# Optimization experiments

Hardware: AMD Instinct MI355X
Metric: run time of the kernel (lower is better)

The kernel has to match this reference:

```python
import jax, jax.numpy as jnp
import numpy as np

B, C, L = 4, 64, 4096
RED = 4          # reduction -> q/k channels = C // RED = 16
N_HASHES = 4
HASH_BUCKETS = min(L // 4, 32)  # = 32, matches torch code
EPS = 1e-5


def _conv1x1(x, W, b):
    # x: [B, Cin, L], W: [Cout, Cin], b: [Cout]
    return jnp.einsum('bcl,oc->bol', x, W) + b[None, :, None]


def setup_inputs() -> dict:
    key = jax.random.key(0)
    ks = jax.random.split(key, 12)
    Cq = C // RED
    x = jax.random.normal(ks[0], (B, C, L), dtype=jnp.float32)
    hash_idx = jax.random.randint(ks[1], (B, N_HASHES, L), 0, HASH_BUCKETS, dtype=jnp.int32)
    sC = 1.0 / np.sqrt(C)
    Wq = jax.random.normal(ks[2], (Cq, C), dtype=jnp.float32) * sC
    bq = jax.random.normal(ks[3], (Cq,), dtype=jnp.float32) * 0.01
    Wk = jax.random.normal(ks[4], (Cq, C), dtype=jnp.float32) * sC
    bk = jax.random.normal(ks[5], (Cq,), dtype=jnp.float32) * 0.01
    Wv = jax.random.normal(ks[6], (C, C), dtype=jnp.float32) * sC
    bv = jax.random.normal(ks[7], (C,), dtype=jnp.float32) * 0.01
    Wo = jax.random.normal(ks[8], (C, C), dtype=jnp.float32) * sC
    bo = jax.random.normal(ks[9], (C,), dtype=jnp.float32) * 0.01
    gamma = jax.random.normal(ks[10], (1,), dtype=jnp.float32)  # nonzero so attn path matters
    bn_w = jnp.ones((C,), dtype=jnp.float32)
    bn_b = jnp.zeros((C,), dtype=jnp.float32)
    return dict(x=x, hash_idx=hash_idx, Wq=Wq, bq=bq, Wk=Wk, bk=bk,
                Wv=Wv, bv=bv, Wo=Wo, bo=bo, gamma=gamma, bn_w=bn_w, bn_b=bn_b)


def reference(x, hash_idx, Wq, bq, Wk, bk, Wv, bv, Wo, bo, gamma, bn_w, bn_b):
    # 1x1 conv projections
    q = _conv1x1(x, Wq, bq)   # [B, C/RED, L]
    k = _conv1x1(x, Wk, bk)   # [B, C/RED, L]
    v = _conv1x1(x, Wv, bv)   # [B, C, L]

    qT = q.transpose(0, 2, 1)  # [B, L, Cq]
    kT = k.transpose(0, 2, 1)
    vT = v.transpose(0, 2, 1)  # [B, L, C]

    # raw scores are hash-independent; only the bucket mask changes per hash
    scores = jnp.einsum('bic,bjc->bij', qT, kT)  # [B, L, L], no sqrt(d) scaling (matches torch)

    n_hashes = hash_idx.shape[1]
    acc = jnp.zeros_like(vT)
    for h in range(n_hashes):  # small fixed loop
        idx = hash_idx[:, h, :]                       # [B, L]
        mask = idx[:, :, None] == idx[:, None, :]     # same-bucket mask [B, L, L]
        s = jnp.where(mask, scores, -1e9)
        attn = jax.nn.softmax(s, axis=-1)             # within-bucket softmax (diag always valid)
        acc = acc + jnp.einsum('bij,bjc->bic', attn, vT)
    attn_out = (acc / n_hashes).transpose(0, 2, 1)    # [B, C, L], averaged over hashes

    out = _conv1x1(attn_out, Wo, bo)
    out = gamma * out + x                             # residual with learned scalar

    # BatchNorm1d, training mode: biased batch stats over (B, L) per channel
    mean = out.mean(axis=(0, 2), keepdims=True)
    var = out.var(axis=(0, 2), keepdims=True)
    out = (out - mean) * jax.lax.rsqrt(var + EPS)
    out = out * bn_w[None, :, None] + bn_b[None, :, None]
    return out
```

## Files before the change

### kernel.cpp

```cpp
#include <hip/hip_runtime.h>
#include <math.h>

#define Bn 4
#define Cn 64
#define Ln 4096
#define CQ 16
#define NH 4
#define NB 32
#define EPSV 1e-5f

#define MAXS 384
#define SFULL 192

#define QSZ   (Bn*Ln*CQ)
#define VSZ   (Bn*Ln*Cn)
#define ACCSZ (Bn*Ln*Cn)
#define NBH   (Bn*NH)

#define OFF_K   QSZ
#define OFF_V   (2*QSZ)
#define OFF_ACC (2*QSZ + VSZ)

#define LOG2E 1.44269504088896f

__global__ __launch_bounds__(256) void proj_kernel(
        const float* __restrict__ x,
        const float* __restrict__ Wq, const float* __restrict__ bq,
        const float* __restrict__ Wk, const float* __restrict__ bk,
        const float* __restrict__ Wv, const float* __restrict__ bv,
        float* __restrict__ q, float* __restrict__ k, float* __restrict__ v) {
    __shared__ float sWt[Cn*32];
    __shared__ float sb[32];
    int tid = threadIdx.x;
    int third = blockIdx.x % 3;
    int pg    = blockIdx.x / 3;
    int rbase = third * 32;
    for (int idx = tid; idx < Cn*32; idx += 256) {
        int rr = idx & 31, c = idx >> 5;
        int r = rbase + rr;
        float w;
        if (r < 16)      w = Wq[r*Cn + c];
        else if (r < 32) w = Wk[(r-16)*Cn + c];
        else             w = Wv[(r-32)*Cn + c];
        sWt[c*32 + rr] = w;
    }
    if (tid < 32) {
        int r = rbase + tid;
        sb[tid] = (r < 16) ? bq[r] : (r < 32 ? bk[r-16] : bv[r-32]);
    }
    __syncthreads();
    int p = tid & 63, og = tid >> 6;
    int gp = pg * 64 + p;
    int b = gp >> 12, l = gp & (Ln - 1);
    const float* xp = &x[b*Cn*Ln + l];
    int rr0 = og * 8;
    float val[8];
    #pragma unroll
    for (int i = 0; i < 8; i++) val[i] = sb[rr0 + i];
    #pragma unroll
    for (int c0 = 0; c0 < Cn; c0 += 8) {
        float xv[8];
        #pragma unroll
        for (int i = 0; i < 8; i++) xv[i] = xp[(c0 + i)*Ln];
        #pragma unroll
        for (int i = 0; i < 8; i++) {
            const float4 wa = *(const float4*)&sWt[(c0 + i)*32 + rr0];
            const float4 wb = *(const float4*)&sWt[(c0 + i)*32 + rr0 + 4];
            float xvi = xv[i];
            val[0] = fmaf(wa.x, xvi, val[0]); val[1] = fmaf(wa.y, xvi, val[1]);
            val[2] = fmaf(wa.z, xvi, val[2]); val[3] = fmaf(wa.w, xvi, val[3]);
            val[4] = fmaf(wb.x, xvi, val[4]); val[5] = fmaf(wb.y, xvi, val[5]);
            val[6] = fmaf(wb.z, xvi, val[6]); val[7] = fmaf(wb.w, xvi, val[7]);
        }
    }
    int f = third*8 + og*2;
    float4 t0 = make_float4(val[0], val[1], val[2], val[3]);
    float4 t1 = make_float4(val[4], val[5], val[6], val[7]);
    float4* q4 = (float4*)&q[gp*CQ];
    float4* k4 = (float4*)&k[gp*CQ];
    float4* v4 = (float4*)&v[gp*Cn];
    if (f < 4)      { q4[f]   = t0; q4[f+1] = t1; }
    else if (f < 8) { k4[f-4] = t0; k4[f-3] = t1; }
    else            { v4[f-8] = t0; v4[f-7] = t1; }
}

__device__ __forceinline__ float quad_reduce_sum(float d) {
    d += __int_as_float(__builtin_amdgcn_mov_dpp(__float_as_int(d), 0xB1, 0xF, 0xF, true));
    d += __int_as_float(__builtin_amdgcn_mov_dpp(__float_as_int(d), 0x4E, 0xF, 0xF, true));
    return d;
}

__device__ __forceinline__ float rowsum16(float x) {
    x += __int_as_float(__builtin_amdgcn_mov_dpp(__float_as_int(x), 0x114, 0xF, 0xF, true));
    x += __int_as_float(__builtin_amdgcn_mov_dpp(__float_as_int(x), 0x118, 0xF, 0xF, true));
    return x;
}

struct SweepState {
    float4 qr[4];
    float4 o[4][4];
    float  lsum[4];
    int    ir[4];
    int    qact[4];
};

__device__ __forceinline__ void sweep_init(SweepState& st, int q0, int S, int act,
        const int* list, const float4* Q4, int qq, int c4) {
    #pragma unroll
    for (int s = 0; s < 4; s++) {
        int qi = q0 + s*4 + qq;
        int a = act && (qi < S);
        st.qact[s] = a;
        int r = a ? list[qi] : 0;
        st.ir[s] = r;
        float4 t = make_float4(0.f, 0.f, 0.f, 0.f);
        if (a) {
            t = Q4[(size_t)r*4 + c4];
            t.x *= LOG2E; t.y *= LOG2E; t.z *= LOG2E; t.w *= LOG2E;
        }
        st.qr[s] = t;
        st.lsum[s] = 0.f;
        #pragma unroll
        for (int tt = 0; tt < 4; tt++) st.o[s][tt] = make_float4(0.f, 0.f, 0.f, 0.f);
    }
}

template<bool MASKED>
__device__ __forceinline__ void kb_step(SweepState& st, int kb, int nkv,
        const float4* ks4, const float4* vs4, int l15, int kk,
        int i0, int i1, int i2, int i3) {
    const float4 kq = ks4[kb*16 + l15];
    const float4 va = vs4[kb*64 + i0*16 + l15];
    const float4 vb = vs4[kb*64 + i1*16 + l15];
    const float4 vc = vs4[kb*64 + i2*16 + l15];
    const float4 vd = vs4[kb*64 + i3*16 + l15];
    #pragma unroll
    for (int s = 0; s < 4; s++) {
        float d = st.qr[s].x * kq.x;
        d = fmaf(st.qr[s].y, kq.y, d);
        d = fmaf(st.qr[s].z, kq.z, d);
        d = fmaf(st.qr[s].w, kq.w, d);
        d = quad_reduce_sum(d);
        float pw = __builtin_amdgcn_exp2f(d);
        if (MASKED) pw = ((kb*4 + kk) < nkv) ? pw : 0.f;
        st.lsum[s] += pw;
        st.o[s][0].x = fmaf(pw, va.x, st.o[s][0].x); st.o[s][0].y = fmaf(pw, va.y, st.o[s][0].y);
        st.o[s][0].z = fmaf(pw, va.z, st.o[s][0].z); st.o[s][0].w = fmaf(pw, va.w, st.o[s][0].w);
        st.o[s][1].x = fmaf(pw, vb.x, st.o[s][1].x); st.o[s][1].y = fmaf(pw, vb.y, st.o[s][1].y);
        st.o[s][1].z = fmaf(pw, vb.z, st.o[s][1].z); st.o[s][1].w = fmaf(pw, vb.w, st.o[s][1].w);
        st.o[s][2].x = fmaf(pw, vc.x, st.o[s][2].x); st.o[s][2].y = fmaf(pw, vc.y, st.o[s][2].y);
        st.o[s][2].z = fmaf(pw, vc.z, st.o[s][2].z); st.o[s][2].w = fmaf(pw, vc.w, st.o[s][2].w);
        st.o[s][3].x = fmaf(pw, vd.x, st.o[s][3].x); st.o[s][3].y = fmaf(pw, vd.y, st.o[s][3].y);
        st.o[s][3].z = fmaf(pw, vd.z, st.o[s][3].z); st.o[s][3].w = fmaf(pw, vd.w, st.o[s][3].w);
    }
}

__device__ __forceinline__ void sweep_keys(SweepState& st, int nk,
        const float4* ks4, const float4* vs4, int l15, int kk,
        int i0, int i1, int i2, int i3) {
    int nf = nk >> 2;
    for (int kb = 0; kb < nf; kb++)
        kb_step<false>(st, kb, nk, ks4, vs4, l15, kk, i0, i1, i2, i3);
    if (nk & 3)
        kb_step<true>(st, nf, nk, ks4, vs4, l15, kk, i0, i1, i2, i3);
}

template<int MODE>
__device__ __forceinline__ void sweep_fin(SweepState& st, float* __restrict__ acc,
        int b, int h, int qq, int lane, int c4) {
    #pragma unroll
    for (int s = 0; s < 4; s++) {
        st.lsum[s] = rowsum16(st.lsum[s]);
        #pragma unroll
        for (int t = 0; t < 4; t++) {
            st.o[s][t].x = rowsum16(st.o[s][t].x);
            st.o[s][t].y = rowsum16(st.o[s][t].y);
            st.o[s][t].z = rowsum16(st.o[s][t].z);
            st.o[s][t].w = rowsum16(st.o[s][t].w);
        }
    }
    if ((lane & 15) < 12) return;
    #pragma unroll
    for (int s = 0; s < 4; s++) {
        if (st.qact[s]) {
            float inv = 1.f / st.lsum[s];
            #pragma unroll
            for (int t = 0; t < 4; t++) {
                float4 r;
                r.x = st.o[s][t].x * inv; r.y = st.o[s][t].y * inv;
                r.z = st.o[s][t].z * inv; r.w = st.o[s][t].w * inv;
                int ch = ((qq + t) & 3)*16 + c4*4;
                if (MODE == 1) {
                    *(float4*)&acc[(((size_t)h*Bn + b)*Ln + st.ir[s])*Cn + ch] = r;
                } else {
                    float* ap = &acc[((size_t)b*Ln + st.ir[s])*Cn + ch];
                    atomicAdd(&ap[0], r.x); atomicAdd(&ap[1], r.y);
                    atomicAdd(&ap[2], r.z); atomicAdd(&ap[3], r.w);
                }
            }
        }
    }
}

__device__ __forceinline__ void stage_kv(int tid, int nk, int k0, const int* list,
        const float4* K4, const float4* V4, float4* ks4, float4* vs4) {
    const float4 z = make_float4(0.f, 0.f, 0.f, 0.f);
    int nb4 = (nk + 3) >> 2;
    for (int G = tid; G < nb4*16; G += 256) {
        int j = G >> 2;
        ks4[G] = (j < nk) ? K4[(size_t)list[k0 + j]*4 + (G & 3)] : z;
    }
    for (int F = tid; F < nb4*64; F += 256) {
        int kb = F >> 6, ii = (F >> 4) & 3, k2 = (F >> 2) & 3, cc = F & 3;
        int j = kb*4 + k2;
        vs4[F] = (j < nk) ? V4[(size_t)list[k0 + j]*16 + ii*4 + cc] : z;
    }
}

template<int MODE>
__global__ __launch_bounds__(256, 2) void attn_kernel(
        const float* __restrict__ q, const float* __restrict__ k,
        const float* __restrict__ v, const int* __restrict__ hidx,
        float* __restrict__ acc) {
    __shared__ int list[MAXS];
    __shared__ int wtot[4];
    __shared__ float4 ks4[SFULL*4];
    __shared__ float4 vs4[SFULL*16];
    int blk = blockIdx.x;
    int u  = blk & (NB-1);
    int bh = blk >> 5;
    int b  = bh >> 2;
    int h  = bh & 3;
    int tid = threadIdx.x;

    const int4* hp4 = (const int4*)(&hidx[bh*Ln] + tid*16);
    int hv[16];
    #pragma unroll
    for (int t = 0; t < 4; t++) {
        int4 tmp = hp4[t];
        hv[t*4+0]=tmp.x; hv[t*4+1]=tmp.y; hv[t*4+2]=tmp.z; hv[t*4+3]=tmp.w;
    }
    int myCnt = 0;
    #pragma unroll
    for (int t = 0; t < 16; t++) myCnt += (hv[t] == u);
    int lane = tid & 63, wv = tid >> 6;
    int pre = myCnt;
    #pragma unroll
    for (int d = 1; d < 64; d <<= 1) {
        int t = __shfl_up(pre, d, 64);
        if (lane >= d) pre += t;
    }
    if (lane == 63) wtot[wv] = pre;
    __syncthreads();
    int base = 0;
    #pragma unroll
    for (int w = 0; w < 4; w++) base += (w < wv) ? wtot[w] : 0;
    int Sall = wtot[0] + wtot[1] + wtot[2] + wtot[3];
    int S = min(Sall, MAXS);
    int excl = base + pre - myCnt;
    #pragma unroll
    for (int t = 0; t < 16; t++) {
        if (hv[t] == u) {
            if (excl < MAXS) list[excl] = tid*16 + t;
            excl++;
        }
    }
    __syncthreads();

    int qq = (lane >> 4) & 3;
    int kk = (lane >> 2) & 3;
    int c4 = lane & 3;
    int l15 = lane & 15;
    int i0 = qq, i1 = (qq+1)&3, i2 = (qq+2)&3, i3 = (qq+3)&3;
    const float4* Q4 = (const float4*)&q[(size_t)b*Ln*CQ];
    const float4* K4 = (const float4*)&k[(size_t)b*Ln*CQ];
    const float4* V4 = (const float4*)&v[(size_t)b*Ln*Cn];

    if (S <= SFULL) {
        stage_kv(tid, S, 0, list, K4, V4, ks4, vs4);
        __syncthreads();
        for (int q0 = wv*16; q0 < S; q0 += 64) {
            SweepState st;
            sweep_init(st, q0, S, 1, list, Q4, qq, c4);
            sweep_keys(st, S, ks4, vs4, l15, kk, i0, i1, i2, i3);
            sweep_fin<MODE>(st, acc, b, h, qq, lane, c4);
        }
    } else {
        for (int q0s = 0; q0s < S; q0s += 64) {
            int q0 = q0s + wv*16;
            int act = q0 < S;
            SweepState st;
            sweep_init(st, q0, S, act, list, Q4, qq, c4);
            for (int k0 = 0; k0 < S; k0 += SFULL) {
                int nk = min(SFULL, S - k0);
                __syncthreads();
                stage_kv(tid, nk, k0, list, K4, V4, ks4, vs4);
                __syncthreads();
                if (act) sweep_keys(st, nk, ks4, vs4, l15, kk, i0, i1, i2, i3);
            }
            if (act) sweep_fin<MODE>(st, acc, b, h, qq, lane, c4);
        }
    }
}

template<int MODE>
__global__ __launch_bounds__(256) void outconv_kernel(
        const float* __restrict__ acc, const float* __restrict__ Wo,
        const float* __restrict__ bo, const float* __restrict__ gamma,
        const float* __restrict__ x, float* __restrict__ y) {
    __shared__ float sWt[Cn*Cn];
    __shared__ float sA[Cn*33];
    __shared__ float sb[Cn];
    int tid = threadIdx.x;
    int pg = blockIdx.x;
    for (int idx = tid; idx < Cn*Cn; idx += 256) {
        int o = idx & 63, c = idx >> 6;
        sWt[c*Cn + o] = Wo[o*Cn + c];
    }
    if (tid < Cn) sb[tid] = bo[tid];
    const float4* a4 = (const float4*)&acc[(size_t)pg*32*Cn];
    #pragma unroll
    for (int r = 0; r < 2; r++) {
        int idx = r*256 + tid;
        int p = idx >> 4, c0 = (idx & 15) * 4;
        float4 t = a4[idx];
        if (MODE == 1) {
            float4 t1 = a4[(size_t)ACCSZ/4   + idx];
            float4 t2 = a4[(size_t)ACCSZ/4*2 + idx];
            float4 t3 = a4[(size_t)ACCSZ/4*3 + idx];
            t.x += t1.x + t2.x + t3.x; t.y += t1.y + t2.y + t3.y;
            t.z += t1.z + t2.z + t3.z; t.w += t1.w + t2.w + t3.w;
        }
        sA[(c0+0)*33 + p] = t.x*0.25f;
        sA[(c0+1)*33 + p] = t.y*0.25f;
        sA[(c0+2)*33 + p] = t.z*0.25f;
        sA[(c0+3)*33 + p] = t.w*0.25f;
    }
    __syncthreads();
    float g = gamma[0];
    int p = tid & 31, og = tid >> 5;
    int gp = pg * 32 + p;
    int b = gp >> 12, l = gp & (Ln - 1);
    int o0 = og * 8;
    float val[8];
    #pragma unroll
    for (int i = 0; i < 8; i++) val[i] = sb[o0 + i];
    #pragma unroll
    for (int c = 0; c < Cn; c++) {
        float av = sA[c*33 + p];
        const float4 wa = *(const float4*)&sWt[c*Cn + o0];
        const float4 wb = *(const float4*)&sWt[c*Cn + o0 + 4];
        val[0] = fmaf(wa.x, av, val[0]); val[1] = fmaf(wa.y, av, val[1]);
        val[2] = fmaf(wa.z, av, val[2]); val[3] = fmaf(wa.w, av, val[3]);
        val[4] = fmaf(wb.x, av, val[4]); val[5] = fmaf(wb.y, av, val[5]);
        val[6] = fmaf(wb.z, av, val[6]); val[7] = fmaf(wb.w, av, val[7]);
    }
    #pragma unroll
    for (int i = 0; i < 8; i++) {
        int o = o0 + i;
        float yv = fmaf(g, val[i], x[(b*Cn + o)*Ln + l]);
        y[(b*Cn + o)*Ln + l] = yv;
    }
}

__global__ __launch_bounds__(256) void stats_kernel(
        const float* __restrict__ y, float* __restrict__ ssumP, float* __restrict__ ssqP) {
    int c = blockIdx.x >> 2;
    int part = blockIdx.x & 3;
    int tid = threadIdx.x;
    const float4* yp = (const float4*)&y[(part*Cn + c)*Ln];
    float s = 0.f, s2 = 0.f;
    #pragma unroll
    for (int i = 0; i < 4; i++) {
        float4 t = yp[i*256 + tid];
        s  += t.x + t.y + t.z + t.w;
        s2 += t.x*t.x + t.y*t.y + t.z*t.z + t.w*t.w;
    }
    #pragma unroll
    for (int w = 1; w < 64; w <<= 1) {
        s  += __shfl_xor(s,  w, 64);
        s2 += __shfl_xor(s2, w, 64);
    }
    __shared__ float rs[4], rs2[4];
    int wv = tid >> 6;
    if ((tid & 63) == 0) { rs[wv] = s; rs2[wv] = s2; }
    __syncthreads();
    if (tid == 0) {
        ssumP[blockIdx.x] = rs[0]+rs[1]+rs[2]+rs[3];
        ssqP[blockIdx.x]  = rs2[0]+rs2[1]+rs2[2]+rs2[3];
    }
}

__global__ __launch_bounds__(256) void norm_kernel(
        const float* __restrict__ y,
        const float* __restrict__ ssumP, const float* __restrict__ ssqP,
        const float* __restrict__ bnw, const float* __restrict__ bnb,
        float* __restrict__ out) {
    int idx = blockIdx.x * 256 + threadIdx.x;
    int flat = idx * 4;
    int c = (flat / Ln) & 63;
    float s = 0.f, s2 = 0.f;
    #pragma unroll
    for (int hh = 0; hh < 4; hh++) { s += ssumP[c*4+hh]; s2 += ssqP[c*4+hh]; }
    const float n = (float)(Bn*Ln);
    float mu = s / n;
    float var = s2 / n - mu*mu;
    float is = rsqrtf(var + EPSV);
    float w = is * bnw[c];
    float bb = bnb[c] - mu * w;
    float4 t = ((const float4*)y)[idx];
    float4 r;
    r.x = t.x*w + bb; r.y = t.y*w + bb; r.z = t.z*w + bb; r.w = t.w*w + bb;
    ((float4*)out)[idx] = r;
}

extern "C" void kernel_launch(void* const* d_in, const int* in_sizes, int n_in,
                              void* d_out, int out_size, void* d_ws, size_t ws_size,
                              hipStream_t stream) {
    const float* x    = (const float*)d_in[0];
    const int*   hidx = (const int*)  d_in[1];
    const float* Wq   = (const float*)d_in[2];
    const float* bq   = (const float*)d_in[3];
    const float* Wk   = (const float*)d_in[4];
    const float* bk   = (const float*)d_in[5];
    const float* Wv   = (const float*)d_in[6];
    const float* bv   = (const float*)d_in[7];
    const float* Wo   = (const float*)d_in[8];
    const float* bo   = (const float*)d_in[9];
    const float* gam  = (const float*)d_in[10];
    const float* bnw  = (const float*)d_in[11];
    const float* bnb  = (const float*)d_in[12];
    float* out = (float*)d_out;

    float* ws  = (float*)d_ws;
    float* q   = ws;
    float* k   = ws + OFF_K;
    float* v   = ws + OFF_V;
    float* acc = ws + OFF_ACC;
    float* y   = ws;

    const size_t bigNeed = ((size_t)OFF_ACC + 4*(size_t)ACCSZ + 512) * sizeof(float);
    bool big = ws_size >= bigNeed;
    float* ssumP = acc + (big ? 4*(size_t)ACCSZ : (size_t)ACCSZ);
    float* ssqP  = ssumP + 256;

    proj_kernel<<<Bn*Ln/64*3, 256, 0, stream>>>(x, Wq, bq, Wk, bk, Wv, bv, q, k, v);
    if (big) {
        attn_kernel<1><<<NBH*NB, 256, 0, stream>>>(q, k, v, hidx, acc);
        outconv_kernel<1><<<Bn*Ln/32, 256, 0, stream>>>(acc, Wo, bo, gam, x, y);
    } else {
        hipMemsetAsync(acc, 0, (size_t)ACCSZ*sizeof(float), stream);
        attn_kernel<0><<<NBH*NB, 256, 0, stream>>>(q, k, v, hidx, acc);
        outconv_kernel<0><<<Bn*Ln/32, 256, 0, stream>>>(acc, Wo, bo, gam, x, y);
    }
    stats_kernel<<<Cn*4, 256, 0, stream>>>(y, ssumP, ssqP);
    norm_kernel<<<Bn*Cn*Ln/4/256, 256, 0, stream>>>(y, ssumP, ssqP, bnw, bnb, out);
}
```

Measured before the change: 157.5 us.

## Fuse BN stats into outconv with atomics and widen attention blocks to 512

```diff
diff --git a/kernel.cpp b/kernel.cpp
--- a/kernel.cpp
+++ b/kernel.cpp
@@ -28,10 +28,12 @@
         const float* __restrict__ Wq, const float* __restrict__ bq,
         const float* __restrict__ Wk, const float* __restrict__ bk,
         const float* __restrict__ Wv, const float* __restrict__ bv,
-        float* __restrict__ q, float* __restrict__ k, float* __restrict__ v) {
+        float* __restrict__ q, float* __restrict__ k, float* __restrict__ v,
+        float* __restrict__ ssum, float* __restrict__ ssq) {
     __shared__ float sWt[Cn*32];
     __shared__ float sb[32];
     int tid = threadIdx.x;
+    if (blockIdx.x == 0 && tid < Cn) { ssum[tid] = 0.f; ssq[tid] = 0.f; }
     int third = blockIdx.x % 3;
     int pg    = blockIdx.x / 3;
     int rbase = third * 32;
@@ -206,11 +208,11 @@
         const float4* K4, const float4* V4, float4* ks4, float4* vs4) {
     const float4 z = make_float4(0.f, 0.f, 0.f, 0.f);
     int nb4 = (nk + 3) >> 2;
-    for (int G = tid; G < nb4*16; G += 256) {
+    for (int G = tid; G < nb4*16; G += 512) {
         int j = G >> 2;
         ks4[G] = (j < nk) ? K4[(size_t)list[k0 + j]*4 + (G & 3)] : z;
     }
-    for (int F = tid; F < nb4*64; F += 256) {
+    for (int F = tid; F < nb4*64; F += 512) {
         int kb = F >> 6, ii = (F >> 4) & 3, k2 = (F >> 2) & 3, cc = F & 3;
         int j = kb*4 + k2;
         vs4[F] = (j < nk) ? V4[(size_t)list[k0 + j]*16 + ii*4 + cc] : z;
@@ -218,12 +220,12 @@
 }
 
 template<int MODE>
-__global__ __launch_bounds__(256, 2) void attn_kernel(
+__global__ __launch_bounds__(512, 4) void attn_kernel(
         const float* __restrict__ q, const float* __restrict__ k,
         const float* __restrict__ v, const int* __restrict__ hidx,
         float* __restrict__ acc) {
     __shared__ int list[MAXS];
-    __shared__ int wtot[4];
+    __shared__ int wtot[8];
     __shared__ float4 ks4[SFULL*4];
     __shared__ float4 vs4[SFULL*16];
     int blk = blockIdx.x;
@@ -233,16 +235,16 @@
     int h  = bh & 3;
     int tid = threadIdx.x;
 
-    const int4* hp4 = (const int4*)(&hidx[bh*Ln] + tid*16);
-    int hv[16];
-    #pragma unroll
-    for (int t = 0; t < 4; t++) {
+    const int4* hp4 = (const int4*)&hidx[bh*Ln + tid*8];
+    int hv[8];
+    #pragma unroll
+    for (int t = 0; t < 2; t++) {
         int4 tmp = hp4[t];
         hv[t*4+0]=tmp.x; hv[t*4+1]=tmp.y; hv[t*4+2]=tmp.z; hv[t*4+3]=tmp.w;
     }
     int myCnt = 0;
     #pragma unroll
-    for (int t = 0; t < 16; t++) myCnt += (hv[t] == u);
+    for (int t = 0; t < 8; t++) myCnt += (hv[t] == u);
     int lane = tid & 63, wv = tid >> 6;
     int pre = myCnt;
     #pragma unroll
@@ -252,16 +254,18 @@
     }
     if (lane == 63) wtot[wv] = pre;
     __syncthreads();
-    int base = 0;
-    #pragma unroll
-    for (int w = 0; w < 4; w++) base += (w < wv) ? wtot[w] : 0;
-    int Sall = wtot[0] + wtot[1] + wtot[2] + wtot[3];
+    int base = 0, Sall = 0;
+    #pragma unroll
+    for (int w = 0; w < 8; w++) {
+        base += (w < wv) ? wtot[w] : 0;
+        Sall += wtot[w];
+    }
     int S = min(Sall, MAXS);
     int excl = base + pre - myCnt;
     #pragma unroll
-    for (int t = 0; t < 16; t++) {
+    for (int t = 0; t < 8; t++) {
         if (hv[t] == u) {
-            if (excl < MAXS) list[excl] = tid*16 + t;
+            if (excl < MAXS) list[excl] = tid*8 + t;
             excl++;
         }
     }
@@ -279,14 +283,14 @@
     if (S <= SFULL) {
         stage_kv(tid, S, 0, list, K4, V4, ks4, vs4);
         __syncthreads();
-        for (int q0 = wv*16; q0 < S; q0 += 64) {
+        for (int q0 = wv*16; q0 < S; q0 += 128) {
             SweepState st;
             sweep_init(st, q0, S, 1, list, Q4, qq, c4);
             sweep_keys(st, S, ks4, vs4, l15, kk, i0, i1, i2, i3);
             sweep_fin<MODE>(st, acc, b, h, qq, lane, c4);
         }
     } else {
-        for (int q0s = 0; q0s < S; q0s += 64) {
+        for (int q0s = 0; q0s < S; q0s += 128) {
             int q0 = q0s + wv*16;
             int act = q0 < S;
             SweepState st;
@@ -307,7 +311,8 @@
 __global__ __launch_bounds__(256) void outconv_kernel(
         const float* __restrict__ acc, const float* __restrict__ Wo,
         const float* __restrict__ bo, const float* __restrict__ gamma,
-        const float* __restrict__ x, float* __restrict__ y) {
+        const float* __restrict__ x, float* __restrict__ y,
+        float* __restrict__ ssum, float* __restrict__ ssq) {
     __shared__ float sWt[Cn*Cn];
     __shared__ float sA[Cn*33];
     __shared__ float sb[Cn];
@@ -355,56 +360,43 @@
         val[4] = fmaf(wb.x, av, val[4]); val[5] = fmaf(wb.y, av, val[5]);
         val[6] = fmaf(wb.z, av, val[6]); val[7] = fmaf(wb.w, av, val[7]);
     }
+    float yv8[8];
     #pragma unroll
     for (int i = 0; i < 8; i++) {
         int o = o0 + i;
         float yv = fmaf(g, val[i], x[(b*Cn + o)*Ln + l]);
         y[(b*Cn + o)*Ln + l] = yv;
-    }
-}
-
-__global__ __launch_bounds__(256) void stats_kernel(
-        const float* __restrict__ y, float* __restrict__ ssumP, float* __restrict__ ssqP) {
-    int c = blockIdx.x >> 2;
-    int part = blockIdx.x & 3;
-    int tid = threadIdx.x;
-    const float4* yp = (const float4*)&y[(part*Cn + c)*Ln];
-    float s = 0.f, s2 = 0.f;
-    #pragma unroll
-    for (int i = 0; i < 4; i++) {
-        float4 t = yp[i*256 + tid];
-        s  += t.x + t.y + t.z + t.w;
-        s2 += t.x*t.x + t.y*t.y + t.z*t.z + t.w*t.w;
-    }
-    #pragma unroll
-    for (int w = 1; w < 64; w <<= 1) {
-        s  += __shfl_xor(s,  w, 64);
-        s2 += __shfl_xor(s2, w, 64);
-    }
-    __shared__ float rs[4], rs2[4];
-    int wv = tid >> 6;
-    if ((tid & 63) == 0) { rs[wv] = s; rs2[wv] = s2; }
-    __syncthreads();
-    if (tid == 0) {
-        ssumP[blockIdx.x] = rs[0]+rs[1]+rs[2]+rs[3];
-        ssqP[blockIdx.x]  = rs2[0]+rs2[1]+rs2[2]+rs2[3];
+        yv8[i] = yv;
+    }
+    __syncthreads();
+    #pragma unroll
+    for (int i = 0; i < 8; i++) sA[(o0+i)*33 + p] = yv8[i];
+    __syncthreads();
+    if (tid < Cn) {
+        int o = tid;
+        float s = 0.f, s2 = 0.f;
+        #pragma unroll 4
+        for (int pp = 0; pp < 32; pp++) {
+            float yv = sA[o*33 + pp];
+            s += yv;
+            s2 = fmaf(yv, yv, s2);
+        }
+        atomicAdd(&ssum[o], s);
+        atomicAdd(&ssq[o], s2);
     }
 }
 
 __global__ __launch_bounds__(256) void norm_kernel(
         const float* __restrict__ y,
-        const float* __restrict__ ssumP, const float* __restrict__ ssqP,
+        const float* __restrict__ ssum, const float* __restrict__ ssq,
         const float* __restrict__ bnw, const float* __restrict__ bnb,
         float* __restrict__ out) {
     int idx = blockIdx.x * 256 + threadIdx.x;
     int flat = idx * 4;
-    int c = (flat / Ln) & 63;
-    float s = 0.f, s2 = 0.f;
-    #pragma unroll
-    for (int hh = 0; hh < 4; hh++) { s += ssumP[c*4+hh]; s2 += ssqP[c*4+hh]; }
+    int c = (flat >> 12) & 63;
     const float n = (float)(Bn*Ln);
-    float mu = s / n;
-    float var = s2 / n - mu*mu;
+    float mu = ssum[c] / n;
+    float var = ssq[c] / n - mu*mu;
     float is = rsqrtf(var + EPSV);
     float w = is * bnw[c];
     float bb = bnb[c] - mu * w;
@@ -441,18 +433,17 @@
 
     const size_t bigNeed = ((size_t)OFF_ACC + 4*(size_t)ACCSZ + 512) * sizeof(float);
     bool big = ws_size >= bigNeed;
-    float* ssumP = acc + (big ? 4*(size_t)ACCSZ : (size_t)ACCSZ);
-    float* ssqP  = ssumP + 256;
-
-    proj_kernel<<<Bn*Ln/64*3, 256, 0, stream>>>(x, Wq, bq, Wk, bk, Wv, bv, q, k, v);
+    float* ssum = acc + (big ? 4*(size_t)ACCSZ : (size_t)ACCSZ);
+    float* ssq  = ssum + 64;
+
+    proj_kernel<<<Bn*Ln/64*3, 256, 0, stream>>>(x, Wq, bq, Wk, bk, Wv, bv, q, k, v, ssum, ssq);
     if (big) {
-        attn_kernel<1><<<NBH*NB, 256, 0, stream>>>(q, k, v, hidx, acc);
-        outconv_kernel<1><<<Bn*Ln/32, 256, 0, stream>>>(acc, Wo, bo, gam, x, y);
+        attn_kernel<1><<<NBH*NB, 512, 0, stream>>>(q, k, v, hidx, acc);
+        outconv_kernel<1><<<Bn*Ln/32, 256, 0, stream>>>(acc, Wo, bo, gam, x, y, ssum, ssq);
     } else {
         hipMemsetAsync(acc, 0, (size_t)ACCSZ*sizeof(float), stream);
-        attn_kernel<0><<<NBH*NB, 256, 0, stream>>>(q, k, v, hidx, acc);
-        outconv_kernel<0><<<Bn*Ln/32, 256, 0, stream>>>(acc, Wo, bo, gam, x, y);
-    }
-    stats_kernel<<<Cn*4, 256, 0, stream>>>(y, ssumP, ssqP);
-    norm_kernel<<<Bn*Cn*Ln/4/256, 256, 0, stream>>>(y, ssumP, ssqP, bnw, bnb, out);
-}
+        attn_kernel<0><<<NBH*NB, 512, 0, stream>>>(q, k, v, hidx, acc);
+        outconv_kernel<0><<<Bn*Ln/32, 256, 0, stream>>>(acc, Wo, bo, gam, x, y, ssum, ssq);
+    }
+    norm_kernel<<<Bn*Cn*Ln/4/256, 256, 0, stream>>>(y, ssum, ssq, bnw, bnb, out);
+}
```

Measured after the change: 171.0 us. +8.6%, slower.
